# Kernel tuning notes

Hardware: AMD Instinct MI355X
Metric: run time of the kernel (lower is better)

The kernel has to match this reference:

```python
import jax, jax.numpy as jnp
import numpy as np
import math

T, B = 1024, 512
DIM_S, DIM_C, DIM_Y = 32, 32, 16
DIM_Z, DIM_H, RANK = 256, 256, 8
ALPHA_Z, ALPHA_H = 0.01, 0.1


def setup_inputs() -> dict:
    key = jax.random.key(0)
    ks = jax.random.split(key, 9)
    return {
        "s": jax.random.normal(ks[0], (T, B, DIM_S), jnp.float32),
        "c": jax.random.normal(ks[1], (T, B, DIM_C), jnp.float32),
        "W_zz": jax.random.normal(ks[2], (DIM_Z, DIM_Z), jnp.float32) * math.sqrt(1.0 / DIM_Z),
        "Wz_in": jax.random.normal(ks[3], (DIM_Z, DIM_S + DIM_C), jnp.float32) * math.sqrt(2.0 / (DIM_Z + DIM_S + DIM_C)),
        "bz_in": jnp.zeros((DIM_Z,), jnp.float32),
        "Wz_out": jax.random.normal(ks[4], (RANK, DIM_Z), jnp.float32) * math.sqrt(2.0 / (RANK + DIM_Z)),
        "bz_out": jnp.zeros((RANK,), jnp.float32),
        "U": jax.random.normal(ks[5], (DIM_H, RANK), jnp.float32) * ((1.0 / DIM_H) ** 0.25 / math.sqrt(RANK)),
        "V": jax.random.normal(ks[6], (DIM_H, RANK), jnp.float32) * ((1.0 / DIM_H) ** 0.25 / math.sqrt(RANK)),
        "W_in": jax.random.normal(ks[7], (DIM_H, DIM_S), jnp.float32) * math.sqrt(2.0 / (DIM_H + DIM_S)),
        "b_in": jnp.zeros((DIM_H,), jnp.float32),
        "W_out": jax.random.normal(ks[8], (DIM_Y, DIM_H), jnp.float32) * math.sqrt(2.0 / (DIM_H + DIM_Y)),
        "b_out": jnp.zeros((DIM_Y,), jnp.float32),
    }


def reference(s, c, W_zz, Wz_in, bz_in, Wz_out, bz_out, U, V, W_in, b_in, W_out, b_out):
    # sig_r = 0 -> noise terms vanish (module default).
    def step(carry, sc_t):
        z, h = carry
        s_t, c_t = sc_t
        tmp = jnp.tanh(z) @ W_zz.T + jnp.concatenate([s_t, c_t], axis=-1) @ Wz_in.T + bz_in
        z = (1.0 - ALPHA_Z) * z + ALPHA_Z * tmp  # [B, Z]
        signal = jax.nn.sigmoid(z @ Wz_out.T + bz_out)  # [B, R]
        # einsum('br,hr,kr,bk->bh') == ((tanh(h) @ V) * signal) @ U.T
        tmp = ((jnp.tanh(h) @ V) * signal) @ U.T + s_t @ W_in.T + b_in
        h = (1.0 - ALPHA_H) * h + ALPHA_H * tmp  # [B, H]
        out = jnp.tanh(h) @ W_out.T + b_out  # [B, Y]
        return (z, h), (out, z, h)

    z0 = jnp.zeros((s.shape[1], DIM_Z), s.dtype)
    h0 = jnp.zeros((s.shape[1], DIM_H), s.dtype)
    _, (outputs, states_z, states_h) = jax.lax.scan(step, (z0, h0), (s, c))
    states = jnp.concatenate([states_z, states_h], axis=-1)  # [T, B, Z+H]
    return outputs, states
```

## Files before the change

### kernel.cpp

```cpp
#include <hip/hip_runtime.h>
#include <math.h>

#define T_STEPS 1024
#define BATCH   512
#define DZ      256
#define DH      256
#define RANK    8
#define DY      16


typedef _Float16 f16;
typedef _Float16 h2 __attribute__((ext_vector_type(2)));

__device__ __forceinline__ h2 pack2(float a, float b) {
    h2 r; r.x = (f16)a; r.y = (f16)b; return r;
}
__device__ __forceinline__ h2 bc(unsigned u) { return __builtin_bit_cast(h2, u); }

__device__ __forceinline__ float dot2(h2 a, h2 b, float c) {
#if __has_builtin(__builtin_amdgcn_fdot2)
    return __builtin_amdgcn_fdot2(a, b, c, false);
#else
    return fmaf((float)a.x, (float)b.x, fmaf((float)a.y, (float)b.y, c));
#endif
}

__device__ __forceinline__ float fast_tanh(float x) {
    const float e = __expf(2.0f * x);
    return 1.0f - 2.0f / (e + 1.0f);
}

__global__ __launch_bounds__(1024, 4)
void nmrnn_kernel(
    const float* __restrict__ s, const float* __restrict__ c,
    const float* __restrict__ W_zz, const float* __restrict__ Wz_in,
    const float* __restrict__ bz_in, const float* __restrict__ Wz_out,
    const float* __restrict__ bz_out, const float* __restrict__ U,
    const float* __restrict__ V, const float* __restrict__ W_in,
    const float* __restrict__ b_in, const float* __restrict__ W_out,
    const float* __restrict__ b_out,
    float* __restrict__ out, float* __restrict__ states)
{
    __shared__ __align__(16) f16 tzh[2][DZ];
    __shared__ __align__(16) f16 thh[2][DH];
    __shared__ __align__(16) f16 sclh[2][64];
    __shared__ __align__(16) float redz[4][2][DZ];
    __shared__ __align__(16) float redh[4][2][DZ];
    __shared__ __align__(16) f16 pz16[RANK][DZ];
    __shared__ __align__(16) f16 pzi16[RANK][64];
    __shared__ __align__(16) f16 vt16[RANK][DH];
    __shared__ __align__(16) f16 ut16[RANK][DH];
    __shared__ __align__(16) f16 wo16[DY][DH];
    __shared__ float gl[2][RANK];
    __shared__ float bo[DY];

    const int tid = threadIdx.x;
    const int i   = tid & 255;
    const int q   = tid >> 8;
    const int l32 = tid & 31;
    const int b0  = blockIdx.x * 2;
    const bool hi = (tid >= 512);

    const int g2 = tid >> 5;
    const int oy = g2 & 15;
    const int ob = g2 >> 4;
    const int gg = g2 & 15;
    const int rr = gg & 7;
    const int rb = gg >> 3;

    h2 wzzp[32];
    #pragma unroll
    for (int m = 0; m < 16; ++m) {
        const float4 v4 = *(const float4*)&W_zz[i * 256 + (q << 6) + (m << 2)];
        wzzp[2 * m]     = pack2(v4.x, v4.y);
        wzzp[2 * m + 1] = pack2(v4.z, v4.w);
    }
    h2 wzip[8];
    #pragma unroll
    for (int m = 0; m < 4; ++m) {
        const float4 v4 = *(const float4*)&Wz_in[i * 64 + (q << 4) + (m << 2)];
        wzip[2 * m]     = pack2(v4.x, v4.y);
        wzip[2 * m + 1] = pack2(v4.z, v4.w);
    }
    h2 wip[4];
    #pragma unroll
    for (int m = 0; m < 2; ++m) {
        const float4 v4 = *(const float4*)&W_in[i * 32 + (q << 3) + (m << 2)];
        wip[2 * m]     = pack2(v4.x, v4.y);
        wip[2 * m + 1] = pack2(v4.z, v4.w);
    }

    {
        const int idx = tid * 4;
        const float4 v4 = *(const float4*)&W_out[idx];
        h2* dst = (h2*)&((f16*)wo16)[idx];
        dst[0] = pack2(v4.x, v4.y);
        dst[1] = pack2(v4.z, v4.w);
    }
    if (tid < 256) {
        #pragma unroll
        for (int r = 0; r < RANK; ++r) vt16[r][tid] = (f16)V[tid * RANK + r];
        #pragma unroll
        for (int r = 0; r < RANK; ++r) ut16[r][tid] = (f16)U[tid * RANK + r];
    }
    if (tid < 512) { tzh[tid >> 8][i] = (f16)0.f; thh[tid >> 8][i] = (f16)0.f; }
    if (tid < DY) bo[tid] = b_out[tid];
    if (tid < 128) {
        const int bb = tid >> 6, r = tid & 63;
        const size_t base = (size_t)(b0 + bb) * 32;
        sclh[bb][r] = (f16)((r < 32) ? s[base + r] : c[base + r - 32]);
    }

    #pragma unroll
    for (int p = 0; p < 2; ++p) {
        const int r = q + 4 * p;
        const float* wrow = &Wz_out[r * 256];
        float a0 = 0.f, a1 = 0.f;
        #pragma unroll 4
        for (int k = 0; k < 256; k += 2) {
            a0 = fmaf(wrow[k],     W_zz[k * 256 + i],       a0);
            a1 = fmaf(wrow[k + 1], W_zz[(k + 1) * 256 + i], a1);
        }
        pz16[r][i] = (f16)(a0 + a1);
    }
    if (tid < 512) {
        const int r = tid >> 6, j = tid & 63;
        const float* wrow = &Wz_out[r * 256];
        float a0 = 0.f, a1 = 0.f;
        #pragma unroll 4
        for (int k = 0; k < 256; k += 2) {
            a0 = fmaf(wrow[k],     Wz_in[k * 64 + j],       a0);
            a1 = fmaf(wrow[k + 1], Wz_in[(k + 1) * 64 + j], a1);
        }
        pzi16[r][j] = (f16)(a0 + a1);
    }

    const float bias_r = hi ? b_in[i] : bz_in[i];
    float state_r = 0.f;

    float czb = 0.f, rzb = 0.f;
    if (hi) {
        float cz = 0.f;
        #pragma unroll
        for (int m = 0; m < 8; ++m) {
            const int k = l32 + 32 * m;
            cz = fmaf(bz_in[k], Wz_out[rr * 256 + k], cz);
        }
        #pragma unroll
        for (int off = 16; off >= 1; off >>= 1) cz += __shfl_xor(cz, off);
        const float bzo_r = bz_out[rr];
        czb = cz + bzo_r;
        rzb = bzo_r;
    }
    __syncthreads();

    for (int t = 0; t < T_STEPS; ++t) {
        float pfn = 0.f;
        if (tid < 128 && t + 1 < T_STEPS) {
            const int bb = tid >> 6, r = tid & 63;
            const size_t base = ((size_t)(t + 1) * BATCH + b0 + bb) * 32;
            pfn = (r < 32) ? s[base + r] : c[base + r - 32];
        }

        if (t > 0) {
            const h2* tp = (const h2*)&thh[ob][0];
            const h2* wp = (const h2*)&wo16[oy][0];
            float o0 = 0.f, o1 = 0.f;
            o0 = dot2(tp[l32],      wp[l32],      o0);
            o1 = dot2(tp[l32 + 32], wp[l32 + 32], o1);
            o0 = dot2(tp[l32 + 64], wp[l32 + 64], o0);
            o1 = dot2(tp[l32 + 96], wp[l32 + 96], o1);
            float o = o0 + o1;
            #pragma unroll
            for (int off = 16; off >= 1; off >>= 1) o += __shfl_xor(o, off);
            if (l32 == 0) out[((size_t)(t - 1) * BATCH + b0 + ob) * 16 + oy] = o + bo[oy];
        }

        if (hi) {
            const h2* tp  = (const h2*)&thh[rb][0];
            const h2* vp  = (const h2*)&vt16[rr][0];
            const h2* tzp = (const h2*)&tzh[rb][0];
            const h2* pzp = (const h2*)&pz16[rr][0];
            float hp0 = 0.f, hp1 = 0.f, zp0 = 0.f, zp1 = 0.f;
            hp0 = dot2(tp[l32],       vp[l32],       hp0);
            hp1 = dot2(tp[l32 + 32],  vp[l32 + 32],  hp1);
            hp0 = dot2(tp[l32 + 64],  vp[l32 + 64],  hp0);
            hp1 = dot2(tp[l32 + 96],  vp[l32 + 96],  hp1);
            zp0 = dot2(tzp[l32],      pzp[l32],      zp0);
            zp1 = dot2(tzp[l32 + 32], pzp[l32 + 32], zp1);
            zp0 = dot2(tzp[l32 + 64], pzp[l32 + 64], zp0);
            zp1 = dot2(tzp[l32 + 96], pzp[l32 + 96], zp1);
            const h2* scp  = (const h2*)&sclh[rb][0];
            const h2* pzip = (const h2*)&pzi16[rr][0];
            zp0 = dot2(scp[l32], pzip[l32], zp0);
            float hp = hp0 + hp1, zp = zp0 + zp1;
            #pragma unroll
            for (int off = 16; off >= 1; off >>= 1) {
                hp += __shfl_xor(hp, off);
                zp += __shfl_xor(zp, off);
            }
            rzb = 0.99f * rzb + 0.01f * (zp + czb);
            const float sg = 1.0f / (1.0f + __expf(-rzb));
            if (l32 == 0) gl[rb][rr] = sg * hp;
        }

        {
            float az0a = 0.f, az0b = 0.f, az1a = 0.f, az1b = 0.f;
            float ah0 = 0.f, ah1 = 0.f;
            const uint4* tz0 = (const uint4*)&tzh[0][q << 6];
            const uint4* tz1 = (const uint4*)&tzh[1][q << 6];
            #pragma unroll
            for (int m = 0; m < 8; ++m) {
                const uint4 u0 = tz0[m];
                const uint4 u1 = tz1[m];
                az0a = dot2(wzzp[4 * m + 0], bc(u0.x), az0a);
                az0a = dot2(wzzp[4 * m + 1], bc(u0.y), az0a);
                az0b = dot2(wzzp[4 * m + 2], bc(u0.z), az0b);
                az0b = dot2(wzzp[4 * m + 3], bc(u0.w), az0b);
                az1a = dot2(wzzp[4 * m + 0], bc(u1.x), az1a);
                az1a = dot2(wzzp[4 * m + 1], bc(u1.y), az1a);
                az1b = dot2(wzzp[4 * m + 2], bc(u1.z), az1b);
                az1b = dot2(wzzp[4 * m + 3], bc(u1.w), az1b);
            }
            const uint4* sp0 = (const uint4*)&sclh[0][q << 4];
            const uint4* sp1 = (const uint4*)&sclh[1][q << 4];
            #pragma unroll
            for (int m = 0; m < 2; ++m) {
                const uint4 u0 = sp0[m];
                const uint4 u1 = sp1[m];
                az0a = dot2(wzip[4 * m + 0], bc(u0.x), az0a);
                az0a = dot2(wzip[4 * m + 1], bc(u0.y), az0a);
                az0b = dot2(wzip[4 * m + 2], bc(u0.z), az0b);
                az0b = dot2(wzip[4 * m + 3], bc(u0.w), az0b);
                az1a = dot2(wzip[4 * m + 0], bc(u1.x), az1a);
                az1a = dot2(wzip[4 * m + 1], bc(u1.y), az1a);
                az1b = dot2(wzip[4 * m + 2], bc(u1.z), az1b);
                az1b = dot2(wzip[4 * m + 3], bc(u1.w), az1b);
            }
            const uint4 uw0 = *(const uint4*)&sclh[0][q << 3];
            const uint4 uw1 = *(const uint4*)&sclh[1][q << 3];
            ah0 = dot2(wip[0], bc(uw0.x), ah0);
            ah0 = dot2(wip[1], bc(uw0.y), ah0);
            ah0 = dot2(wip[2], bc(uw0.z), ah0);
            ah0 = dot2(wip[3], bc(uw0.w), ah0);
            ah1 = dot2(wip[0], bc(uw1.x), ah1);
            ah1 = dot2(wip[1], bc(uw1.y), ah1);
            ah1 = dot2(wip[2], bc(uw1.z), ah1);
            ah1 = dot2(wip[3], bc(uw1.w), ah1);
            redz[q][0][i] = az0a + az0b;
            redz[q][1][i] = az1a + az1b;
            redh[q][0][i] = ah0;
            redh[q][1][i] = ah1;
        }
        __syncthreads();

        if (!hi) {
            const int bb = q;
            const float tmp = redz[0][bb][i] + redz[1][bb][i]
                            + redz[2][bb][i] + redz[3][bb][i] + bias_r;
            state_r = 0.99f * state_r + 0.01f * tmp;
            tzh[bb][i] = (f16)fast_tanh(state_r);
            states[((size_t)t * BATCH + b0 + bb) * 512 + i] = state_r;
        } else {
            const int bb = q - 2;
            float t0 = redh[0][bb][i] + redh[1][bb][i]
                     + redh[2][bb][i] + redh[3][bb][i] + bias_r;
            float t1 = 0.f;
            #pragma unroll
            for (int r = 0; r < 4; ++r) {
                t0 = fmaf((float)ut16[2 * r][i],     gl[bb][2 * r],     t0);
                t1 = fmaf((float)ut16[2 * r + 1][i], gl[bb][2 * r + 1], t1);
            }
            state_r = 0.9f * state_r + 0.1f * (t0 + t1);
            thh[bb][i] = (f16)fast_tanh(state_r);
            states[((size_t)t * BATCH + b0 + bb) * 512 + 256 + i] = state_r;
        }
        if (tid < 128 && t + 1 < T_STEPS)
            sclh[tid >> 6][tid & 63] = (f16)pfn;
        __syncthreads();
    }

    {
        const h2* tp = (const h2*)&thh[ob][0];
        const h2* wp = (const h2*)&wo16[oy][0];
        float o0 = 0.f, o1 = 0.f;
        o0 = dot2(tp[l32],      wp[l32],      o0);
        o1 = dot2(tp[l32 + 32], wp[l32 + 32], o1);
        o0 = dot2(tp[l32 + 64], wp[l32 + 64], o0);
        o1 = dot2(tp[l32 + 96], wp[l32 + 96], o1);
        float o = o0 + o1;
        #pragma unroll
        for (int off = 16; off >= 1; off >>= 1) o += __shfl_xor(o, off);
        if (l32 == 0)
            out[((size_t)(T_STEPS - 1) * BATCH + b0 + ob) * 16 + oy] = o + bo[oy];
    }
}

extern "C" void kernel_launch(void* const* d_in, const int* in_sizes, int n_in,
                              void* d_out, int out_size, void* d_ws, size_t ws_size,
                              hipStream_t stream) {
    const float* s     = (const float*)d_in[0];
    const float* c     = (const float*)d_in[1];
    const float* W_zz  = (const float*)d_in[2];
    const float* Wz_in = (const float*)d_in[3];
    const float* bz_in = (const float*)d_in[4];
    const float* Wz_out= (const float*)d_in[5];
    const float* bz_out= (const float*)d_in[6];
    const float* U     = (const float*)d_in[7];
    const float* V     = (const float*)d_in[8];
    const float* W_in  = (const float*)d_in[9];
    const float* b_in  = (const float*)d_in[10];
    const float* W_out = (const float*)d_in[11];
    const float* b_out = (const float*)d_in[12];

    float* out    = (float*)d_out;
    float* states = out + (size_t)T_STEPS * BATCH * DY;

    hipLaunchKernelGGL(nmrnn_kernel, dim3(BATCH / 2), dim3(1024), 0, stream,
                       s, c, W_zz, Wz_in, bz_in, Wz_out, bz_out, U, V,
                       W_in, b_in, W_out, b_out, out, states);
}
```

Baseline: 2.265 ms.

## Process one batch element per block instead of two, doubling grid size

```diff
diff --git a/kernel.cpp b/kernel.cpp
--- a/kernel.cpp
+++ b/kernel.cpp
@@ -41,32 +41,29 @@
     const float* __restrict__ b_out,
     float* __restrict__ out, float* __restrict__ states)
 {
-    __shared__ __align__(16) f16 tzh[2][DZ];
-    __shared__ __align__(16) f16 thh[2][DH];
-    __shared__ __align__(16) f16 sclh[2][64];
-    __shared__ __align__(16) float redz[4][2][DZ];
-    __shared__ __align__(16) float redh[4][2][DZ];
+    __shared__ __align__(16) f16 tzh[DZ];
+    __shared__ __align__(16) f16 thh[DH];
+    __shared__ __align__(16) f16 sclh[64];
+    __shared__ __align__(16) float redz[4][DZ];
+    __shared__ __align__(16) float redh[4][DZ];
     __shared__ __align__(16) f16 pz16[RANK][DZ];
     __shared__ __align__(16) f16 pzi16[RANK][64];
     __shared__ __align__(16) f16 vt16[RANK][DH];
     __shared__ __align__(16) f16 ut16[RANK][DH];
     __shared__ __align__(16) f16 wo16[DY][DH];
-    __shared__ float gl[2][RANK];
+    __shared__ float gl[RANK];
     __shared__ float bo[DY];
 
     const int tid = threadIdx.x;
     const int i   = tid & 255;
     const int q   = tid >> 8;
+    const int w   = tid >> 6;
     const int l32 = tid & 31;
-    const int b0  = blockIdx.x * 2;
-    const bool hi = (tid >= 512);
-
-    const int g2 = tid >> 5;
-    const int oy = g2 & 15;
-    const int ob = g2 >> 4;
-    const int gg = g2 & 15;
-    const int rr = gg & 7;
-    const int rb = gg >> 3;
+    const int b   = blockIdx.x;
+
+    const int oy = (tid >> 5) & 15;
+    const int rr = (tid >> 5) & 7;
+    const int px = tid & 63;
 
     h2 wzzp[32];
     #pragma unroll
@@ -102,13 +99,12 @@
         for (int r = 0; r < RANK; ++r) vt16[r][tid] = (f16)V[tid * RANK + r];
         #pragma unroll
         for (int r = 0; r < RANK; ++r) ut16[r][tid] = (f16)U[tid * RANK + r];
-    }
-    if (tid < 512) { tzh[tid >> 8][i] = (f16)0.f; thh[tid >> 8][i] = (f16)0.f; }
+        tzh[tid] = (f16)0.f; thh[tid] = (f16)0.f;
+    }
     if (tid < DY) bo[tid] = b_out[tid];
-    if (tid < 128) {
-        const int bb = tid >> 6, r = tid & 63;
-        const size_t base = (size_t)(b0 + bb) * 32;
-        sclh[bb][r] = (f16)((r < 32) ? s[base + r] : c[base + r - 32]);
+    if (tid < 64) {
+        const size_t base = (size_t)b * 32;
+        sclh[tid] = (f16)((tid < 32) ? s[base + tid] : c[base + tid - 32]);
     }
 
     #pragma unroll
@@ -135,11 +131,12 @@
         pzi16[r][j] = (f16)(a0 + a1);
     }
 
-    const float bias_r = hi ? b_in[i] : bz_in[i];
+    const float bias_r = (tid < 256) ? bz_in[i]
+                       : (tid < 512) ? b_in[i] : 0.f;
     float state_r = 0.f;
 
     float czb = 0.f, rzb = 0.f;
-    if (hi) {
+    if (w >= 8 && w < 12) {
         float cz = 0.f;
         #pragma unroll
         for (int m = 0; m < 8; ++m) {
@@ -156,30 +153,29 @@
 
     for (int t = 0; t < T_STEPS; ++t) {
         float pfn = 0.f;
-        if (tid < 128 && t + 1 < T_STEPS) {
-            const int bb = tid >> 6, r = tid & 63;
-            const size_t base = ((size_t)(t + 1) * BATCH + b0 + bb) * 32;
-            pfn = (r < 32) ? s[base + r] : c[base + r - 32];
-        }
-
-        if (t > 0) {
-            const h2* tp = (const h2*)&thh[ob][0];
-            const h2* wp = (const h2*)&wo16[oy][0];
-            float o0 = 0.f, o1 = 0.f;
-            o0 = dot2(tp[l32],      wp[l32],      o0);
-            o1 = dot2(tp[l32 + 32], wp[l32 + 32], o1);
-            o0 = dot2(tp[l32 + 64], wp[l32 + 64], o0);
-            o1 = dot2(tp[l32 + 96], wp[l32 + 96], o1);
-            float o = o0 + o1;
-            #pragma unroll
-            for (int off = 16; off >= 1; off >>= 1) o += __shfl_xor(o, off);
-            if (l32 == 0) out[((size_t)(t - 1) * BATCH + b0 + ob) * 16 + oy] = o + bo[oy];
-        }
-
-        if (hi) {
-            const h2* tp  = (const h2*)&thh[rb][0];
+        if (w >= 12 && px < 64 && tid < 832 && t + 1 < T_STEPS) {
+            const size_t base = ((size_t)(t + 1) * BATCH + b) * 32;
+            pfn = (px < 32) ? s[base + px] : c[base + px - 32];
+        }
+
+        if (w < 8) {
+            if (t > 0) {
+                const h2* tp = (const h2*)thh;
+                const h2* wp = (const h2*)&wo16[oy][0];
+                float o0 = 0.f, o1 = 0.f;
+                o0 = dot2(tp[l32],      wp[l32],      o0);
+                o1 = dot2(tp[l32 + 32], wp[l32 + 32], o1);
+                o0 = dot2(tp[l32 + 64], wp[l32 + 64], o0);
+                o1 = dot2(tp[l32 + 96], wp[l32 + 96], o1);
+                float o = o0 + o1;
+                #pragma unroll
+                for (int off = 16; off >= 1; off >>= 1) o += __shfl_xor(o, off);
+                if (l32 == 0) out[((size_t)(t - 1) * BATCH + b) * 16 + oy] = o + bo[oy];
+            }
+        } else if (w < 12) {
+            const h2* tp  = (const h2*)thh;
             const h2* vp  = (const h2*)&vt16[rr][0];
-            const h2* tzp = (const h2*)&tzh[rb][0];
+            const h2* tzp = (const h2*)tzh;
             const h2* pzp = (const h2*)&pz16[rr][0];
             float hp0 = 0.f, hp1 = 0.f, zp0 = 0.f, zp1 = 0.f;
             hp0 = dot2(tp[l32],       vp[l32],       hp0);
@@ -190,7 +186,7 @@
             zp1 = dot2(tzp[l32 + 32], pzp[l32 + 32], zp1);
             zp0 = dot2(tzp[l32 + 64], pzp[l32 + 64], zp0);
             zp1 = dot2(tzp[l32 + 96], pzp[l32 + 96], zp1);
-            const h2* scp  = (const h2*)&sclh[rb][0];
+            const h2* scp  = (const h2*)sclh;
             const h2* pzip = (const h2*)&pzi16[rr][0];
             zp0 = dot2(scp[l32], pzip[l32], zp0);
             float hp = hp0 + hp1, zp = zp0 + zp1;
@@ -201,87 +197,65 @@
             }
             rzb = 0.99f * rzb + 0.01f * (zp + czb);
             const float sg = 1.0f / (1.0f + __expf(-rzb));
-            if (l32 == 0) gl[rb][rr] = sg * hp;
+            if (l32 == 0) gl[rr] = sg * hp;
         }
 
         {
-            float az0a = 0.f, az0b = 0.f, az1a = 0.f, az1b = 0.f;
-            float ah0 = 0.f, ah1 = 0.f;
-            const uint4* tz0 = (const uint4*)&tzh[0][q << 6];
-            const uint4* tz1 = (const uint4*)&tzh[1][q << 6];
+            float aza = 0.f, azb = 0.f, ah = 0.f;
+            const uint4* tz = (const uint4*)&tzh[q << 6];
             #pragma unroll
             for (int m = 0; m < 8; ++m) {
-                const uint4 u0 = tz0[m];
-                const uint4 u1 = tz1[m];
-                az0a = dot2(wzzp[4 * m + 0], bc(u0.x), az0a);
-                az0a = dot2(wzzp[4 * m + 1], bc(u0.y), az0a);
-                az0b = dot2(wzzp[4 * m + 2], bc(u0.z), az0b);
-                az0b = dot2(wzzp[4 * m + 3], bc(u0.w), az0b);
-                az1a = dot2(wzzp[4 * m + 0], bc(u1.x), az1a);
-                az1a = dot2(wzzp[4 * m + 1], bc(u1.y), az1a);
-                az1b = dot2(wzzp[4 * m + 2], bc(u1.z), az1b);
-                az1b = dot2(wzzp[4 * m + 3], bc(u1.w), az1b);
-            }
-            const uint4* sp0 = (const uint4*)&sclh[0][q << 4];
-            const uint4* sp1 = (const uint4*)&sclh[1][q << 4];
+                const uint4 u = tz[m];
+                aza = dot2(wzzp[4 * m + 0], bc(u.x), aza);
+                aza = dot2(wzzp[4 * m + 1], bc(u.y), aza);
+                azb = dot2(wzzp[4 * m + 2], bc(u.z), azb);
+                azb = dot2(wzzp[4 * m + 3], bc(u.w), azb);
+            }
+            const uint4* sp = (const uint4*)&sclh[q << 4];
             #pragma unroll
             for (int m = 0; m < 2; ++m) {
-                const uint4 u0 = sp0[m];
-                const uint4 u1 = sp1[m];
-                az0a = dot2(wzip[4 * m + 0], bc(u0.x), az0a);
-                az0a = dot2(wzip[4 * m + 1], bc(u0.y), az0a);
-                az0b = dot2(wzip[4 * m + 2], bc(u0.z), az0b);
-                az0b = dot2(wzip[4 * m + 3], bc(u0.w), az0b);
-                az1a = dot2(wzip[4 * m + 0], bc(u1.x), az1a);
-                az1a = dot2(wzip[4 * m + 1], bc(u1.y), az1a);
-                az1b = dot2(wzip[4 * m + 2], bc(u1.z), az1b);
-                az1b = dot2(wzip[4 * m + 3], bc(u1.w), az1b);
-            }
-            const uint4 uw0 = *(const uint4*)&sclh[0][q << 3];
-            const uint4 uw1 = *(const uint4*)&sclh[1][q << 3];
-            ah0 = dot2(wip[0], bc(uw0.x), ah0);
-            ah0 = dot2(wip[1], bc(uw0.y), ah0);
-            ah0 = dot2(wip[2], bc(uw0.z), ah0);
-            ah0 = dot2(wip[3], bc(uw0.w), ah0);
-            ah1 = dot2(wip[0], bc(uw1.x), ah1);
-            ah1 = dot2(wip[1], bc(uw1.y), ah1);
-            ah1 = dot2(wip[2], bc(uw1.z), ah1);
-            ah1 = dot2(wip[3], bc(uw1.w), ah1);
-            redz[q][0][i] = az0a + az0b;
-            redz[q][1][i] = az1a + az1b;
-            redh[q][0][i] = ah0;
-            redh[q][1][i] = ah1;
+                const uint4 u = sp[m];
+                aza = dot2(wzip[4 * m + 0], bc(u.x), aza);
+                aza = dot2(wzip[4 * m + 1], bc(u.y), aza);
+                azb = dot2(wzip[4 * m + 2], bc(u.z), azb);
+                azb = dot2(wzip[4 * m + 3], bc(u.w), azb);
+            }
+            const uint4 uw = *(const uint4*)&sclh[q << 3];
+            ah = dot2(wip[0], bc(uw.x), ah);
+            ah = dot2(wip[1], bc(uw.y), ah);
+            ah = dot2(wip[2], bc(uw.z), ah);
+            ah = dot2(wip[3], bc(uw.w), ah);
+            redz[q][i] = aza + azb;
+            redh[q][i] = ah;
         }
         __syncthreads();
 
-        if (!hi) {
-            const int bb = q;
-            const float tmp = redz[0][bb][i] + redz[1][bb][i]
-                            + redz[2][bb][i] + redz[3][bb][i] + bias_r;
+        if (tid < 256) {
+            const float tmp = redz[0][i] + redz[1][i]
+                            + redz[2][i] + redz[3][i] + bias_r;
             state_r = 0.99f * state_r + 0.01f * tmp;
-            tzh[bb][i] = (f16)fast_tanh(state_r);
-            states[((size_t)t * BATCH + b0 + bb) * 512 + i] = state_r;
-        } else {
-            const int bb = q - 2;
-            float t0 = redh[0][bb][i] + redh[1][bb][i]
-                     + redh[2][bb][i] + redh[3][bb][i] + bias_r;
+            tzh[i] = (f16)fast_tanh(state_r);
+            states[((size_t)t * BATCH + b) * 512 + i] = state_r;
+        } else if (tid < 512) {
+            float t0 = redh[0][i] + redh[1][i]
+                     + redh[2][i] + redh[3][i] + bias_r;
             float t1 = 0.f;
             #pragma unroll
             for (int r = 0; r < 4; ++r) {
-                t0 = fmaf((float)ut16[2 * r][i],     gl[bb][2 * r],     t0);
-                t1 = fmaf((float)ut16[2 * r + 1][i], gl[bb][2 * r + 1], t1);
+                t0 = fmaf((float)ut16[2 * r][i],     gl[2 * r],     t0);
+                t1 = fmaf((float)ut16[2 * r + 1][i], gl[2 * r + 1], t1);
             }
             state_r = 0.9f * state_r + 0.1f * (t0 + t1);
-            thh[bb][i] = (f16)fast_tanh(state_r);
-            states[((size_t)t * BATCH + b0 + bb) * 512 + 256 + i] = state_r;
-        }
-        if (tid < 128 && t + 1 < T_STEPS)
-            sclh[tid >> 6][tid & 63] = (f16)pfn;
+            thh[i] = (f16)fast_tanh(state_r);
+            states[((size_t)t * BATCH + b) * 512 + 256 + i] = state_r;
+        }
+        if (w >= 12 && px < 64 && tid < 832 && t + 1 < T_STEPS)
+            sclh[px] = (f16)pfn;
         __syncthreads();
     }
 
-    {
-        const h2* tp = (const h2*)&thh[ob][0];
+    if (w < 8) {
+        const h2* tp = (const h2*)thh;
         const h2* wp = (const h2*)&wo16[oy][0];
         float o0 = 0.f, o1 = 0.f;
         o0 = dot2(tp[l32],      wp[l32],      o0);
@@ -292,7 +266,7 @@
         #pragma unroll
         for (int off = 16; off >= 1; off >>= 1) o += __shfl_xor(o, off);
         if (l32 == 0)
-            out[((size_t)(T_STEPS - 1) * BATCH + b0 + ob) * 16 + oy] = o + bo[oy];
+            out[((size_t)(T_STEPS - 1) * BATCH + b) * 16 + oy] = o + bo[oy];
     }
 }
 
@@ -316,7 +290,7 @@
     float* out    = (float*)d_out;
     float* states = out + (size_t)T_STEPS * BATCH * DY;
 
-    hipLaunchKernelGGL(nmrnn_kernel, dim3(BATCH / 2), dim3(1024), 0, stream,
+    hipLaunchKernelGGL(nmrnn_kernel, dim3(BATCH), dim3(1024), 0, stream,
                        s, c, W_zz, Wz_in, bz_in, Wz_out, bz_out, U, V,
                        W_in, b_in, W_out, b_out, out, states);
 }
```

Result: slower. 3.052 ms (+34.7%).
